# Kernel tuning notes

Measured on AMD Instinct MI355X. Metric: run time of the kernel, lower is better.

The kernel has to match this reference:

```python
import jax, jax.numpy as jnp
import numpy as np

HC = 64                 # half_context
PAD = HC + 3            # padding_idx row of positional table
NEG = 1.0e12            # additive mask constant from the torch code


def setup_inputs() -> dict:
    key = jax.random.key(0)
    ks = jax.random.split(key, 7)
    B, S, D, C = 32, 2048, 1024, 256
    embeds = jax.random.normal(ks[0], (B, S, D), dtype=jnp.float32)
    embeds_mask = jnp.ones((B, S), dtype=jnp.float32)
    latent = jax.random.normal(ks[1], (C, D), dtype=jnp.float32)
    att_diag = jax.random.normal(ks[2], (D,), dtype=jnp.float32)
    tok_diag = jax.random.normal(ks[3], (D,), dtype=jnp.float32)
    pos_table = jax.random.normal(ks[4], (2 * HC + 4, D), dtype=jnp.float32)
    pos_table = pos_table.at[PAD].set(0.0)  # padding_idx row is zeros
    tok_mult = jnp.ones((1,), dtype=jnp.float32)
    rel_pos_ids = jax.random.randint(ks[5], (B, S), 0, HC + 4, dtype=jnp.int32)
    return {
        "embeds": embeds,
        "embeds_mask": embeds_mask,
        "latent": latent,
        "att_diag": att_diag,
        "tok_diag": tok_diag,
        "pos_table": pos_table,
        "tok_mult": tok_mult,
        "rel_pos_ids": rel_pos_ids,
    }


def reference(embeds, embeds_mask, latent, att_diag, tok_diag, pos_table, tok_mult, rel_pos_ids):
    # positional-embedding gather and merge (dropouts are identity in eval)
    absolute_pos = rel_pos_ids + HC                       # [B,S]
    pos_embeds = pos_table[absolute_pos]                  # [B,S,D]
    merged = tok_mult[0] * embeds + pos_embeds            # [B,S,D]
    # entity-token attention scores: (latent * diag) @ merged^T
    scores = jnp.einsum('cd,bsd->bcs', latent * att_diag, merged)  # [B,C,S]
    m = embeds_mask[:, None, :]                           # [B,1,S]
    scores = scores * m + (m - 1.0) * NEG                 # mask-add
    top = jnp.max(scores, axis=1)                         # max over classes -> [B,S]
    att_probs = jax.nn.softmax(top, axis=1)               # softmax over tokens
    # weighted sum of (embeds * tok_diag) by attention probs -> [B,D]
    ctx_vecs = jnp.einsum('bsd,d,bs->bd', embeds, tok_diag, att_probs)
    return ctx_vecs
```

## Files before the change

### kernel.cpp

```cpp
#include <hip/hip_runtime.h>
#include <hip/hip_bf16.h>


#define HC 64
#define NEGV 1000000000000.0f

constexpr int Bb = 32, Ss = 2048, Dd = 1024, Cc = 256;
constexpr int NKC = 32;
constexpr int CT = Cc / 16;
constexpr int NBLK = 16;

typedef _Float16 f16x8 __attribute__((ext_vector_type(8)));
typedef float    f32x4 __attribute__((ext_vector_type(4)));

__global__ __launch_bounds__(256) void k_prep_w(
    const float* __restrict__ latent, const float* __restrict__ att_diag,
    _Float16* __restrict__ whi)
{
    const int idx = blockIdx.x * 256 + threadIdx.x;
    const int c = idx >> 10, k = idx & 1023;
    const float wv = latent[idx] * att_diag[k];
    const int kc = k >> 5, g = (k >> 3) & 3, i = k & 7;
    const int lane = (c & 15) + 16 * g, ct = c >> 4;
    whi[(size_t)kc * 8192 + (size_t)ct * 512 + lane * 8 + i] = (_Float16)wv;
}

__global__ __launch_bounds__(256, 2) void k_scores_mfma(
    const float* __restrict__ embeds,
    const float* __restrict__ mask,
    const float* __restrict__ pos_table,
    const float* __restrict__ tok_mult,
    const int*   __restrict__ rel_ids,
    const _Float16* __restrict__ whi,
    float* __restrict__ partial,
    float* __restrict__ mblk,
    float* __restrict__ zblk)
{
    __shared__ _Float16 sbuf[2][8192];
    __shared__ float l_sh[128];
    __shared__ float w_sh[128];
    __shared__ float red2[2], zred[2];

    const int t  = threadIdx.x;
    const int wv = t >> 6;
    const int l  = t & 63;
    const int lr = l & 15;
    const int lg = l >> 4;

    const int b   = blockIdx.x >> 4;
    const int blk = blockIdx.x & 15;
    const int s0  = blk * 128;

    const float tm = tok_mult[0];

    const float* erow[2];
    const float* prow[2];
    #pragma unroll
    for (int st = 0; st < 2; st++) {
        const int tok = s0 + wv * 32 + st * 16 + lr;
        erow[st] = embeds + ((size_t)b * Ss + tok) * Dd;
        prow[st] = pos_table + (size_t)(rel_ids[b * Ss + tok] + HC) * Dd;
    }

    f32x4 acc[CT][2];
    #pragma unroll
    for (int ct = 0; ct < CT; ct++)
        #pragma unroll
        for (int st = 0; st < 2; st++) acc[ct][st] = (f32x4){0.f, 0.f, 0.f, 0.f};

    f32x4 e0[2], e1[2], p0[2], p1[2];
    auto loadEP = [&](int kc) {
        const int k0 = kc * 32 + lg * 8;
        #pragma unroll
        for (int st = 0; st < 2; st++) {
            e0[st] = *(const f32x4*)(erow[st] + k0);
            e1[st] = *(const f32x4*)(erow[st] + k0 + 4);
            p0[st] = *(const f32x4*)(prow[st] + k0);
            p1[st] = *(const f32x4*)(prow[st] + k0 + 4);
        }
    };

    auto stage = [&](int kc, _Float16* dst) {
        const _Float16* src = whi + (size_t)kc * 8192;
        #pragma unroll
        for (int i = 0; i < 4; i++) {
            const int off = (i * 4 + wv) << 9;
            __builtin_amdgcn_global_load_lds(
                (const __attribute__((address_space(1))) void*)(src + off + l * 8),
                (__attribute__((address_space(3))) void*)(dst + off),
                16, 0, 0);
        }
    };

    stage(0, sbuf[0]);
    loadEP(0);
    asm volatile("s_waitcnt vmcnt(8)" ::: "memory");
    __builtin_amdgcn_s_barrier();

    int cur = 0;
    for (int kc = 0; kc < NKC; kc++) {
        if (kc + 1 < NKC) stage(kc + 1, sbuf[cur ^ 1]);

        f16x8 bh[2], bl[2];
        #pragma unroll
        for (int st = 0; st < 2; st++) {
            float e[8], p[8];
            *(f32x4*)&e[0] = e0[st]; *(f32x4*)&e[4] = e1[st];
            *(f32x4*)&p[0] = p0[st]; *(f32x4*)&p[4] = p1[st];
            #pragma unroll
            for (int i = 0; i < 8; i++) {
                const float x = fmaf(tm, e[i], p[i]);
                const _Float16 h = (_Float16)x;
                bh[st][i] = h;
                bl[st][i] = (_Float16)(x - (float)h);
            }
        }
        if (kc + 1 < NKC) loadEP(kc + 1);

        const _Float16* base = sbuf[cur];
        #pragma unroll
        for (int ct = 0; ct < CT; ct++) {
            const f16x8 ah = *(const f16x8*)(base + ct * 512 + l * 8);
            #pragma unroll
            for (int st = 0; st < 2; st++) {
                acc[ct][st] = __builtin_amdgcn_mfma_f32_16x16x32_f16(ah, bh[st], acc[ct][st], 0, 0, 0);
                acc[ct][st] = __builtin_amdgcn_mfma_f32_16x16x32_f16(ah, bl[st], acc[ct][st], 0, 0, 0);
            }
        }
        if (kc + 1 < NKC) { asm volatile("s_waitcnt vmcnt(8)" ::: "memory"); }
        else              { asm volatile("s_waitcnt vmcnt(0)" ::: "memory"); }
        __builtin_amdgcn_s_barrier();
        cur ^= 1;
    }

    #pragma unroll
    for (int st = 0; st < 2; st++) {
        float mx = acc[0][st][0];
        #pragma unroll
        for (int ct = 0; ct < CT; ct++)
            #pragma unroll
            for (int r = 0; r < 4; r++) mx = fmaxf(mx, acc[ct][st][r]);
        mx = fmaxf(mx, __shfl_xor(mx, 16));
        mx = fmaxf(mx, __shfl_xor(mx, 32));
        if (lg == 0) {
            const int si = wv * 32 + st * 16 + lr;
            const int s  = s0 + si;
            const float mk = mask[b * Ss + s];
            l_sh[si] = mx * mk + (mk - 1.0f) * NEGV;
        }
    }
    __syncthreads();

    if (t < 128) {
        float v = l_sh[t];
        #pragma unroll
        for (int o = 32; o >= 1; o >>= 1) v = fmaxf(v, __shfl_xor(v, o));
        if ((t & 63) == 0) red2[t >> 6] = v;
    }
    __syncthreads();
    const float Mb = fmaxf(red2[0], red2[1]);
    if (t < 128) w_sh[t] = expf(l_sh[t] - Mb);
    __syncthreads();
    if (t < 128) {
        float z = w_sh[t];
        #pragma unroll
        for (int o = 32; o >= 1; o >>= 1) z += __shfl_xor(z, o);
        if ((t & 63) == 0) zred[t >> 6] = z;
    }
    __syncthreads();

    {
        const float* eb = embeds + ((size_t)b * Ss + s0) * Dd + t * 4;
        f32x4 ca = (f32x4){0.f, 0.f, 0.f, 0.f};
        #pragma unroll 8
        for (int s = 0; s < 128; s++) {
            const float wgt = w_sh[s];
            const f32x4 ev = *(const f32x4*)(eb + (size_t)s * Dd);
            ca[0] = fmaf(wgt, ev[0], ca[0]);
            ca[1] = fmaf(wgt, ev[1], ca[1]);
            ca[2] = fmaf(wgt, ev[2], ca[2]);
            ca[3] = fmaf(wgt, ev[3], ca[3]);
        }
        *(f32x4*)(partial + ((size_t)(b * NBLK + blk)) * Dd + t * 4) = ca;
        if (t == 0) {
            mblk[b * NBLK + blk] = Mb;
            zblk[b * NBLK + blk] = zred[0] + zred[1];
        }
    }
}

__global__ __launch_bounds__(256) void k_finish(
    const float* __restrict__ mblk, const float* __restrict__ zblk,
    const float* __restrict__ partial, const float* __restrict__ tok_diag,
    float* __restrict__ out)
{
    __shared__ float cf[NBLK];
    const int b  = blockIdx.x >> 2;
    const int dq = blockIdx.x & 3;
    const int t  = threadIdx.x;

    if (t < 64) {
        const float mv = (t < NBLK) ? mblk[b * NBLK + t] : -3.4e38f;
        float M = mv;
        #pragma unroll
        for (int o = 32; o >= 1; o >>= 1) M = fmaxf(M, __shfl_xor(M, o));
        const float zv = (t < NBLK) ? zblk[b * NBLK + t] * expf(mv - M) : 0.f;
        float Z = zv;
        #pragma unroll
        for (int o = 32; o >= 1; o >>= 1) Z += __shfl_xor(Z, o);
        if (t < NBLK) cf[t] = expf(mv - M) / Z;
    }
    __syncthreads();

    const int d = dq * 256 + t;
    float a = 0.f;
    #pragma unroll
    for (int j = 0; j < NBLK; j++)
        a = fmaf(cf[j], partial[((size_t)(b * NBLK + j)) * Dd + d], a);
    out[(size_t)b * Dd + d] = a * tok_diag[d];
}

extern "C" void kernel_launch(void* const* d_in, const int* in_sizes, int n_in,
                              void* d_out, int out_size, void* d_ws, size_t ws_size,
                              hipStream_t stream) {
    const float* embeds    = (const float*)d_in[0];
    const float* mask      = (const float*)d_in[1];
    const float* latent    = (const float*)d_in[2];
    const float* att_diag  = (const float*)d_in[3];
    const float* tok_diag  = (const float*)d_in[4];
    const float* pos_table = (const float*)d_in[5];
    const float* tok_mult  = (const float*)d_in[6];
    const int*   rel_ids   = (const int*)d_in[7];
    float* out = (float*)d_out;

    char* ws = (char*)d_ws;
    _Float16* whi    = (_Float16*)(ws);
    float*    partial= (float*)(ws + 524288);
    float*    mblk   = (float*)(ws + 2621440);
    float*    zblk   = (float*)(ws + 2623488);

    k_prep_w<<<(Cc * Dd) / 256, 256, 0, stream>>>(latent, att_diag, whi);
    k_scores_mfma<<<Bb * NBLK, 256, 0, stream>>>(
        embeds, mask, pos_table, tok_mult, rel_ids, whi, partial, mblk, zblk);
    k_finish<<<Bb * 4, 256, 0, stream>>>(mblk, zblk, partial, tok_diag, out);
}
```

Measured before the change: 121.4 us.

## Stage embeds tiles into LDS via async global_load_lds with XOR swizzle

Embeds rows are no longer loaded per-lane into registers. Each k-chunk of the 128x32 fp32 embeds tile is now staged into a double-buffered LDS buffer with direct global-to-LDS loads, using an XOR swizzle so reads avoid bank conflicts. The goal is more coalesced global access and lower register pressure, with the embeds loads overlapped with the MFMA work on the previous chunk. The cost is 32KB more LDS per block, which may reduce occupancy below the two-blocks-per-CU launch bound, and the vmcnt bookkeeping gets more fragile.

```diff
diff --git a/kernel.cpp b/kernel.cpp
--- a/kernel.cpp
+++ b/kernel.cpp
@@ -36,7 +36,8 @@
     float* __restrict__ mblk,
     float* __restrict__ zblk)
 {
-    __shared__ _Float16 sbuf[2][8192];
+    __shared__ _Float16 sbufW[2][8192];
+    __shared__ float    sbufE[2][4096];
     __shared__ float l_sh[128];
     __shared__ float w_sh[128];
     __shared__ float red2[2], zred[2];
@@ -53,12 +54,10 @@
 
     const float tm = tok_mult[0];
 
-    const float* erow[2];
     const float* prow[2];
     #pragma unroll
     for (int st = 0; st < 2; st++) {
         const int tok = s0 + wv * 32 + st * 16 + lr;
-        erow[st] = embeds + ((size_t)b * Ss + tok) * Dd;
         prow[st] = pos_table + (size_t)(rel_ids[b * Ss + tok] + HC) * Dd;
     }
 
@@ -68,19 +67,17 @@
         #pragma unroll
         for (int st = 0; st < 2; st++) acc[ct][st] = (f32x4){0.f, 0.f, 0.f, 0.f};
 
-    f32x4 e0[2], e1[2], p0[2], p1[2];
-    auto loadEP = [&](int kc) {
+    f32x4 p0[2], p1[2];
+    auto loadP = [&](int kc) {
         const int k0 = kc * 32 + lg * 8;
         #pragma unroll
         for (int st = 0; st < 2; st++) {
-            e0[st] = *(const f32x4*)(erow[st] + k0);
-            e1[st] = *(const f32x4*)(erow[st] + k0 + 4);
             p0[st] = *(const f32x4*)(prow[st] + k0);
             p1[st] = *(const f32x4*)(prow[st] + k0 + 4);
         }
     };
 
-    auto stage = [&](int kc, _Float16* dst) {
+    auto stageW = [&](int kc, _Float16* dst) {
         const _Float16* src = whi + (size_t)kc * 8192;
         #pragma unroll
         for (int i = 0; i < 4; i++) {
@@ -92,32 +89,58 @@
         }
     };
 
-    stage(0, sbuf[0]);
-    loadEP(0);
-    asm volatile("s_waitcnt vmcnt(8)" ::: "memory");
+    auto stageE = [&](int kc, float* dst) {
+        const float* ebase = embeds + ((size_t)b * Ss + s0) * Dd + kc * 32;
+        #pragma unroll
+        for (int i = 0; i < 4; i++) {
+            const int jbase = i * 256 + wv * 64;
+            const int j = jbase + l;
+            const int row = j >> 3, u = j & 7;
+            const float* src = ebase + (size_t)row * Dd + ((u ^ (row & 7)) << 2);
+            __builtin_amdgcn_global_load_lds(
+                (const __attribute__((address_space(1))) void*)src,
+                (__attribute__((address_space(3))) void*)(dst + jbase * 4),
+                16, 0, 0);
+        }
+    };
+
+    stageW(0, sbufW[0]);
+    stageE(0, sbufE[0]);
+    loadP(0);
+    asm volatile("s_waitcnt vmcnt(4)" ::: "memory");
     __builtin_amdgcn_s_barrier();
 
     int cur = 0;
     for (int kc = 0; kc < NKC; kc++) {
-        if (kc + 1 < NKC) stage(kc + 1, sbuf[cur ^ 1]);
+        if (kc + 1 < NKC) {
+            stageW(kc + 1, sbufW[cur ^ 1]);
+            stageE(kc + 1, sbufE[cur ^ 1]);
+        }
 
         f16x8 bh[2], bl[2];
-        #pragma unroll
-        for (int st = 0; st < 2; st++) {
-            float e[8], p[8];
-            *(f32x4*)&e[0] = e0[st]; *(f32x4*)&e[4] = e1[st];
-            *(f32x4*)&p[0] = p0[st]; *(f32x4*)&p[4] = p1[st];
+        {
+            const float* es = sbufE[cur];
             #pragma unroll
-            for (int i = 0; i < 8; i++) {
-                const float x = fmaf(tm, e[i], p[i]);
-                const _Float16 h = (_Float16)x;
-                bh[st][i] = h;
-                bl[st][i] = (_Float16)(x - (float)h);
+            for (int st = 0; st < 2; st++) {
+                const int row = wv * 32 + st * 16 + lr;
+                const int sw  = row & 7;
+                const f32x4 x0 = *(const f32x4*)(es + row * 32 + (((lg << 1)    ) ^ sw) * 4);
+                const f32x4 x1 = *(const f32x4*)(es + row * 32 + (((lg << 1) | 1) ^ sw) * 4);
+                float e[8], p[8];
+                *(f32x4*)&e[0] = x0;     *(f32x4*)&e[4] = x1;
+                *(f32x4*)&p[0] = p0[st]; *(f32x4*)&p[4] = p1[st];
+                #pragma unroll
+                for (int i = 0; i < 8; i++) {
+                    const float x = fmaf(tm, e[i], p[i]);
+                    const _Float16 h = (_Float16)x;
+                    bh[st][i] = h;
+                    bl[st][i] = (_Float16)(x - (float)h);
+                }
             }
         }
-        if (kc + 1 < NKC) loadEP(kc + 1);
-
-        const _Float16* base = sbuf[cur];
+        if (kc + 1 < NKC) loadP(kc + 1);
+
+        const _Float16* base = sbufW[cur];
         #pragma unroll
         for (int ct = 0; ct < CT; ct++) {
             const f16x8 ah = *(const f16x8*)(base + ct * 512 + l * 8);
@@ -127,7 +150,7 @@
                 acc[ct][st] = __builtin_amdgcn_mfma_f32_16x16x32_f16(ah, bl[st], acc[ct][st], 0, 0, 0);
             }
         }
-        if (kc + 1 < NKC) { asm volatile("s_waitcnt vmcnt(8)" ::: "memory"); }
+        if (kc + 1 < NKC) { asm volatile("s_waitcnt vmcnt(4)" ::: "memory"); }
         else              { asm volatile("s_waitcnt vmcnt(0)" ::: "memory"); }
         __builtin_amdgcn_s_barrier();
         cur ^= 1;
```

Measured after the change: 113.6 us. -6.4%, faster.
